# Kernel tuning notes

Hardware: AMD Instinct MI355X
Metric: run time of the kernel (lower is better)

## Reference

```python
import jax, jax.numpy as jnp
import numpy as np

N_NODES = 100000
N_EDGES = 1000000
D = 64  # gat_input_size == gat_hidden_size
NEG_SLOPE = 0.2  # PyG GATConv default leaky_relu slope


def setup_inputs() -> dict:
    key = jax.random.key(0)
    k1, k2, k3, k4, k5, k6 = jax.random.split(key, 6)
    g = jax.random.normal(k1, (N_NODES, D), dtype=jnp.float32)
    edge_index = jax.random.randint(k2, (2, N_EDGES), 0, N_NODES, dtype=jnp.int32)
    scale = 1.0 / np.sqrt(D)
    W = jax.random.normal(k3, (D, D), dtype=jnp.float32) * scale
    att_src = jax.random.normal(k4, (D,), dtype=jnp.float32) * scale
    att_dst = jax.random.normal(k5, (D,), dtype=jnp.float32) * scale
    bias = jnp.zeros((D,), dtype=jnp.float32)
    return {"g": g, "edge_index": edge_index, "W": W,
            "att_src": att_src, "att_dst": att_dst, "bias": bias}


def _gat_layer(x, src, dst, W, att_src, att_dst, bias):
    N = x.shape[0]
    h = x @ W                               # [N, D] projected features
    a_src = h @ att_src                     # [N] per-node source logits
    a_dst = h @ att_dst                     # [N] per-node target logits
    e = jax.nn.leaky_relu(a_src[src] + a_dst[dst], NEG_SLOPE)  # [E]
    # numerically stable segment softmax over edges grouped by target node
    m = jax.ops.segment_max(e, dst, num_segments=N)            # [N]
    m = jnp.where(jnp.isfinite(m), m, 0.0)                     # isolated nodes
    ex = jnp.exp(e - m[dst])                                   # [E]
    denom = jax.ops.segment_sum(ex, dst, num_segments=N)       # [N]
    alpha = ex / (denom[dst] + 1e-16)                          # [E]
    out = jax.ops.segment_sum(alpha[:, None] * h[src], dst, num_segments=N)
    return out + bias


def reference(g, edge_index, W, att_src, att_dst, bias):
    src, dst = edge_index[0], edge_index[1]
    for _ in range(4):  # same shared GAT applied 4 times
        g = _gat_layer(g, src, dst, W, att_src, att_dst, bias)
    return g
```

## Files before the change

kernel.cpp:

```cpp
#include <hip/hip_runtime.h>
#include <hip/hip_bf16.h>

typedef unsigned int u32;
typedef unsigned short u16;
typedef unsigned long long u64;
typedef __attribute__((ext_vector_type(8))) short short8;
typedef __attribute__((ext_vector_type(4))) float f32x4;
typedef __attribute__((ext_vector_type(2))) float f32x2;

#define LRELU_SLOPE 0.2f
#define BPB 32
#define MAXPER 13000

__device__ inline float bfbits(u32 hi) { union { u32 i; float f; } v; v.i = hi; return v.f; }
__device__ inline float bflo(u32 w) { return bfbits(w << 16); }
__device__ inline float bfhi(u32 w) { return bfbits(w & 0xFFFF0000u); }
__device__ inline float bf2f(u16 s) { return bfbits(((u32)s) << 16); }
__device__ inline u16 f2bf(float f) {
  union { float f; u32 i; } v; v.f = f;
  u32 r = v.i + 0x7FFFu + ((v.i >> 16) & 1u);
  return (u16)(r >> 16);
}
__device__ inline f32x2 up2(u32 w) { return (f32x2){bflo(w), bfhi(w)}; }

__global__ void dp_kernel(const u32* __restrict__ g, int nwords, int* __restrict__ mode,
                          const void* __restrict__ W, const void* __restrict__ as,
                          const void* __restrict__ ad, const void* __restrict__ bs,
                          float* __restrict__ pf, u16* __restrict__ wfrag,
                          int* __restrict__ gcnt) {
  __shared__ int cnt;
  if (threadIdx.x == 0) cnt = 0;
  if (threadIdx.x < 8) gcnt[threadIdx.x] = 0;
  __syncthreads();
  int c = 0;
  for (int i = threadIdx.x; i < nwords; i += 256) {
    u32 e = g[i] & 0x7F80u;
    if (e >= 0x3000u && e <= 0x4180u) c++;
  }
  atomicAdd(&cnt, c);
  __syncthreads();
  int md = (2 * cnt > nwords) ? 1 : 0;
  if (threadIdx.x == 0) *mode = md;

  for (int i = threadIdx.x; i < 4288; i += 256) {
    const void* p; int j;
    if (i < 4096)      { p = W;  j = i; }
    else if (i < 4160) { p = as; j = i - 4096; }
    else if (i < 4224) { p = ad; j = i - 4160; }
    else               { p = bs; j = i - 4224; }
    pf[i] = md ? bf2f(((const u16*)p)[j]) : ((const float*)p)[j];
  }
  __syncthreads();
  for (int i = threadIdx.x; i < 4096; i += 256) {
    int f = i >> 9, lane = (i >> 3) & 63, j = i & 7;
    int cc = f >> 1, t = f & 1;
    int k = 32 * t + 8 * (lane >> 4) + j;
    int n = 16 * cc + (lane & 15);
    wfrag[i] = f2bf(pf[k * 64 + n]);
  }
}

__global__ void __launch_bounds__(256) binA_kernel(
    const int* __restrict__ src, const int* __restrict__ dst, int* __restrict__ gcnt,
    uint2* __restrict__ binned, int E, int nper, int cap) {
  __shared__ int lcnt[8], lbase[8], lcur[8];
  const int K = 8;
  int tile0 = blockIdx.x * (256 * K);
  int t = threadIdx.x;
  if (t < 8) { lcnt[t] = 0; lcur[t] = 0; }
  __syncthreads();
  int dv[K], sv[K], bv[K];
#pragma unroll
  for (int j = 0; j < K; ++j) {
    int idx = tile0 + j * 256 + t;
    bool ok = idx < E;
    int d = ok ? __builtin_nontemporal_load(&dst[idx]) : 0;
    int s = ok ? __builtin_nontemporal_load(&src[idx]) : 0;
    int b = -1;
    if (ok) {
      b = (d >= 4 * nper) ? 4 : 0;
      if (d >= (b + 2) * nper) b += 2;
      if (d >= (b + 1) * nper) b += 1;
      atomicAdd(&lcnt[b], 1);
    }
    dv[j] = d; sv[j] = s; bv[j] = b;
  }
  __syncthreads();
  if (t < 8) lbase[t] = atomicAdd(&gcnt[t], lcnt[t]);
  __syncthreads();
#pragma unroll
  for (int j = 0; j < K; ++j) {
    int b = bv[j];
    if (b >= 0) {
      int slot = lbase[b] + atomicAdd(&lcur[b], 1);
      if (slot < cap) binned[(size_t)b * cap + slot] = make_uint2((u32)sv[j], (u32)dv[j]);
    }
  }
}

__global__ void __launch_bounds__(256) histA_kernel(
    const uint2* __restrict__ binned, const int* __restrict__ gcnt,
    u32* __restrict__ slices, int nper, int cap) {
  __shared__ u32 cnt_lds[MAXPER];
  int b = blockIdx.x & 7;
  int j = blockIdx.x >> 3;
  int cnt = gcnt[b]; if (cnt > cap) cnt = cap;
  int chunk = (cnt + BPB - 1) / BPB;
  int begin = j * chunk;
  int endc = begin + chunk; if (endc > cnt) endc = cnt;
  for (int k = threadIdx.x; k < nper; k += 256) cnt_lds[k] = 0;
  __syncthreads();
  const uint2* reg = binned + (size_t)b * cap;
  int kbase = b * nper;
  for (int i = begin + threadIdx.x; i < endc; i += 256)
    atomicAdd(&cnt_lds[(int)reg[i].y - kbase], 1u);
  __syncthreads();
  u32* out = slices + (size_t)(b * BPB + j) * nper;
  for (int k = threadIdx.x; k < nper; k += 256) out[k] = cnt_lds[k];
}

__global__ void scan1f_kernel(const u32* __restrict__ slices, int* __restrict__ row_off,
                              int* __restrict__ partials, int nper, int N) {
  __shared__ int smem[1024];
  int t = threadIdx.x;
  int idx = blockIdx.x * 1024 + t;
  int v = 0;
  if (idx < N) {
    int b = idx / nper;
    int kk = idx - b * nper;
    const u32* s = slices + (size_t)b * BPB * nper + kk;
    u32 tt = 0;
#pragma unroll 8
    for (int j = 0; j < BPB; ++j) tt += s[(size_t)j * nper];
    v = (int)((tt + 7u) & ~7u);
  }
  smem[t] = v;
  __syncthreads();
  for (int off = 1; off < 1024; off <<= 1) {
    int u = (t >= off) ? smem[t - off] : 0;
    __syncthreads();
    smem[t] += u;
    __syncthreads();
  }
  if (idx < N) row_off[idx + 1] = smem[t];
  if (t == 1023) partials[blockIdx.x] = smem[t];
}

__global__ void scan3c_kernel(int* __restrict__ row_off, const int* __restrict__ partials,
                              int P, u32* __restrict__ slices, int* __restrict__ csr_src,
                              int nper, int N, int dummy) {
  __shared__ int smem[1024];
  int t = threadIdx.x;
  int pv = (t < P) ? partials[t] : 0;
  smem[t] = pv;
  __syncthreads();
  for (int off = 1; off < 1024; off <<= 1) {
    int u = (t >= off) ? smem[t - off] : 0;
    __syncthreads();
    smem[t] += u;
    __syncthreads();
  }
  int blk = blockIdx.x;
  int prefix = (blk > 0) ? smem[blk - 1] : 0;
  int idx = blk * 1024 + t;
  if (idx == 0) row_off[0] = 0;
  if (idx < N) {
    int vend = row_off[idx + 1] + prefix;
    row_off[idx + 1] = vend;
    int b = idx / nper;
    int kk = idx - b * nper;
    u32* s = slices + (size_t)b * BPB * nper + kk;
    u32 tv[BPB];
    u32 deg = 0;
#pragma unroll
    for (int j = 0; j < BPB; ++j) { tv[j] = s[(size_t)j * nper]; deg += tv[j]; }
    u32 pdeg = (deg + 7u) & ~7u;
    u32 run = (u32)vend - pdeg;
#pragma unroll
    for (int j = 0; j < BPB; ++j) { s[(size_t)j * nper] = run; run += tv[j]; }
    for (u32 p = run; p < (u32)vend; ++p) csr_src[p] = dummy;
  }
}

__global__ void __launch_bounds__(256) scatterB_kernel(
    const uint2* __restrict__ binned, const int* __restrict__ gcnt,
    const u32* __restrict__ slices, int* __restrict__ csr_src, int nper, int cap) {
  __shared__ u32 base_lds[MAXPER];
  int b = blockIdx.x & 7;
  int j = blockIdx.x >> 3;
  int cnt = gcnt[b]; if (cnt > cap) cnt = cap;
  int chunk = (cnt + BPB - 1) / BPB;
  int begin = j * chunk;
  int endc = begin + chunk; if (endc > cnt) endc = cnt;
  const u32* s = slices + (size_t)(b * BPB + j) * nper;
  for (int k = threadIdx.x; k < nper; k += 256) base_lds[k] = s[k];
  __syncthreads();
  const uint2* reg = binned + (size_t)b * cap;
  int kbase = b * nper;
  for (int i = begin + threadIdx.x; i < endc; i += 256) {
    uint2 r = reg[i];
    u32 p = atomicAdd(&base_lds[(int)r.y - kbase], 1u);
    csr_src[p] = (int)r.x;
  }
}

__global__ void hist_local_kernel(const uint2* __restrict__ binned, const int* __restrict__ gcnt,
                                  int* __restrict__ deg, int cap) {
  int b = blockIdx.x & 7;
  int vb = blockIdx.x >> 3, nvb = gridDim.x >> 3;
  int cnt = gcnt[b]; if (cnt > cap) cnt = cap;
  const uint2* reg = binned + (size_t)b * cap;
  for (int i = vb * blockDim.x + threadIdx.x; i < cnt; i += nvb * blockDim.x)
    atomicAdd(&deg[reg[i].y], 1);
}

__global__ void scatter_local_kernel(const uint2* __restrict__ binned, const int* __restrict__ gcnt,
                                     int* __restrict__ cursor, int* __restrict__ csr_src, int cap) {
  int b = blockIdx.x & 7;
  int vb = blockIdx.x >> 3, nvb = gridDim.x >> 3;
  int cnt = gcnt[b]; if (cnt > cap) cnt = cap;
  const uint2* reg = binned + (size_t)b * cap;
  for (int i = vb * blockDim.x + threadIdx.x; i < cnt; i += nvb * blockDim.x) {
    uint2 r = reg[i];
    int p = atomicAdd(&cursor[r.y], 1);
    csr_src[p] = (int)r.x;
  }
}

__global__ void scan1_kernel(const int* __restrict__ deg, int* __restrict__ row_off,
                             int* __restrict__ partials, int N) {
  __shared__ int smem[1024];
  int t = threadIdx.x;
  int idx = blockIdx.x * 1024 + t;
  int v = (idx < N) ? (int)(((u32)deg[idx] + 7u) & ~7u) : 0;
  smem[t] = v;
  __syncthreads();
  for (int off = 1; off < 1024; off <<= 1) {
    int u = (t >= off) ? smem[t - off] : 0;
    __syncthreads();
    smem[t] += u;
    __syncthreads();
  }
  if (idx < N) row_off[idx + 1] = smem[t];
  if (t == 1023) partials[blockIdx.x] = smem[t];
}

__global__ void scan2_kernel(int* __restrict__ partials, int P) {
  __shared__ int smem[1024];
  int t = threadIdx.x;
  int v = (t < P) ? partials[t] : 0;
  smem[t] = v;
  __syncthreads();
  for (int off = 1; off < 1024; off <<= 1) {
    int u = (t >= off) ? smem[t - off] : 0;
    __syncthreads();
    smem[t] += u;
    __syncthreads();
  }
  if (t < P) partials[t] = smem[t];
}

__global__ void scan3_kernel(int* __restrict__ row_off, const int* __restrict__ partials,
                             int* __restrict__ cursor, int N) {
  int b = blockIdx.x;
  int idx = b * 1024 + threadIdx.x;
  if (idx < N) {
    int v = row_off[idx + 1] + ((b > 0) ? partials[b - 1] : 0);
    row_off[idx + 1] = v;
    if (idx + 1 < N) cursor[idx + 1] = v;
  }
  if (idx == 0) { row_off[0] = 0; cursor[0] = 0; }
}

__global__ void padC_kernel(const int* __restrict__ row_off, const int* __restrict__ cursor,
                            int* __restrict__ csr_src, int N, int dummy) {
  int i = blockIdx.x * blockDim.x + threadIdx.x;
  if (i >= N) return;
  int e = row_off[i + 1];
  for (int p = cursor[i]; p < e; ++p) csr_src[p] = dummy;
}

__global__ void __launch_bounds__(256) proj_mfma_kernel(
    const u16* __restrict__ x, const void* __restrict__ graw, const int* __restrict__ mode,
    int first, const u16* __restrict__ wfrag, const float* __restrict__ pf,
    u16* __restrict__ h, float* __restrict__ a_src, float* __restrict__ a_dst, int N) {
  if (blockIdx.x == 0) {
    if (threadIdx.x < 32) ((u32*)(h + (size_t)N * 64))[threadIdx.x] = 0u;
    else if (threadIdx.x == 32) a_src[N] = -1e30f;
  }
  int lane = threadIdx.x & 63;
  int quad = lane >> 4, m = lane & 15;
  int wtile = (int)((blockIdx.x * (size_t)blockDim.x + threadIdx.x) >> 6);
  int ntiles = (N + 15) >> 4;
  int nwaves = (int)((gridDim.x * (size_t)blockDim.x) >> 6);

  int md = *mode;
  bool f32in = (first && md == 0);
  const u16* xin = (first && md) ? (const u16*)graw : x;

  short8 bfrag[8];
#pragma unroll
  for (int f = 0; f < 8; ++f)
    bfrag[f] = *(const short8*)(wfrag + f * 512 + lane * 8);
  float asv[4], adv[4];
#pragma unroll
  for (int c = 0; c < 4; ++c) {
    asv[c] = pf[4096 + 16 * c + m];
    adv[c] = pf[4160 + 16 * c + m];
  }

  for (int tile = wtile; tile < ntiles; tile += nwaves) {
    int row0 = tile << 4;
    int rl = row0 + m; if (rl > N - 1) rl = N - 1;
    short8 a0, a1;
    if (f32in) {
      const float* xr = (const float*)graw + (size_t)rl * 64 + 8 * quad;
      float4 f0 = *(const float4*)(xr);
      float4 f1 = *(const float4*)(xr + 4);
      float4 f2 = *(const float4*)(xr + 32);
      float4 f3 = *(const float4*)(xr + 36);
      a0[0] = (short)f2bf(f0.x); a0[1] = (short)f2bf(f0.y);
      a0[2] = (short)f2bf(f0.z); a0[3] = (short)f2bf(f0.w);
      a0[4] = (short)f2bf(f1.x); a0[5] = (short)f2bf(f1.y);
      a0[6] = (short)f2bf(f1.z); a0[7] = (short)f2bf(f1.w);
      a1[0] = (short)f2bf(f2.x); a1[1] = (short)f2bf(f2.y);
      a1[2] = (short)f2bf(f2.z); a1[3] = (short)f2bf(f2.w);
      a1[4] = (short)f2bf(f3.x); a1[5] = (short)f2bf(f3.y);
      a1[6] = (short)f2bf(f3.z); a1[7] = (short)f2bf(f3.w);
    } else {
      const u16* xr = xin + (size_t)rl * 64 + 8 * quad;
      a0 = *(const short8*)(xr);
      a1 = *(const short8*)(xr + 32);
    }

    f32x4 acc[4];
#pragma unroll
    for (int c = 0; c < 4; ++c) {
      f32x4 z = {0.f, 0.f, 0.f, 0.f};
      z = __builtin_amdgcn_mfma_f32_16x16x32_bf16(a0, bfrag[2 * c + 0], z, 0, 0, 0);
      z = __builtin_amdgcn_mfma_f32_16x16x32_bf16(a1, bfrag[2 * c + 1], z, 0, 0, 0);
      acc[c] = z;
    }

#pragma unroll
    for (int r = 0; r < 4; ++r) {
      int row = row0 + 4 * quad + r;
      float v0 = acc[0][r], v1 = acc[1][r], v2 = acc[2][r], v3 = acc[3][r];
      if (row < N) {
        u16* hr = h + (size_t)row * 64 + m;
        hr[0]  = f2bf(v0);
        hr[16] = f2bf(v1);
        hr[32] = f2bf(v2);
        hr[48] = f2bf(v3);
      }
      float s1 = v0 * asv[0] + v1 * asv[1] + v2 * asv[2] + v3 * asv[3];
      float s2 = v0 * adv[0] + v1 * adv[1] + v2 * adv[2] + v3 * adv[3];
#pragma unroll
      for (int msk = 1; msk <= 8; msk <<= 1) {
        s1 += __shfl_xor(s1, msk, 64);
        s2 += __shfl_xor(s2, msk, 64);
      }
      if (m == 0 && row < N) { a_src[row] = s1; a_dst[row] = s2; }
    }
  }
}

__global__ void __launch_bounds__(256) gather_kernel(
    const u16* __restrict__ h, const float* __restrict__ a_src,
    const float* __restrict__ a_dst, const int* __restrict__ row_off,
    const int* __restrict__ csr_src, const float* __restrict__ pf,
    u16* __restrict__ xout, void* __restrict__ dout, int N, int last,
    const int* __restrict__ mode) {
  int lane = threadIdx.x & 63;
  int grp = lane >> 4;
  int eg  = (lane >> 3) & 1;
  int fg  = lane & 7;
  int wid = (int)((blockIdx.x * blockDim.x + threadIdx.x) >> 6);
  int i0 = wid * 4;
  if (i0 >= N) return;
  int i = i0 + grp;
  bool valid = i < N;

  int beg = 0, end = 0;
  float adv = 0.f;
  if (valid) {
    beg = row_off[i];
    end = row_off[i + 1];
    adv = a_dst[i];
  }

  f32x2 acc0 = {0.f, 0.f}, acc1 = {0.f, 0.f}, acc2 = {0.f, 0.f}, acc3 = {0.f, 0.f};
  float den = 0.f;

  for (int b0 = beg; b0 < end; b0 += 8) {
    int eA = b0 + eg;
    int sA = csr_src[eA];
    int sB = csr_src[eA + 2];
    int sC = csr_src[eA + 4];
    int sD = csr_src[eA + 6];
    float aA = a_src[sA];
    float aB = a_src[sB];
    float aC = a_src[sC];
    float aD = a_src[sD];
    uint4 hA = ((const uint4*)(h + (size_t)sA * 64))[fg];
    uint4 hB = ((const uint4*)(h + (size_t)sB * 64))[fg];
    uint4 hC = ((const uint4*)(h + (size_t)sC * 64))[fg];
    uint4 hD = ((const uint4*)(h + (size_t)sD * 64))[fg];

    float tA = aA + adv; tA = (tA > 0.f) ? tA : LRELU_SLOPE * tA;
    float tB = aB + adv; tB = (tB > 0.f) ? tB : LRELU_SLOPE * tB;
    float tC = aC + adv; tC = (tC > 0.f) ? tC : LRELU_SLOPE * tC;
    float tD = aD + adv; tD = (tD > 0.f) ? tD : LRELU_SLOPE * tD;
    float wA = __expf(fminf(tA, 60.f));
    float wB = __expf(fminf(tB, 60.f));
    float wC = __expf(fminf(tC, 60.f));
    float wD = __expf(fminf(tD, 60.f));
    den += (wA + wB) + (wC + wD);
    f32x2 wA2 = {wA, wA}, wB2 = {wB, wB}, wC2 = {wC, wC}, wD2 = {wD, wD};
    acc0 += wA2 * up2(hA.x); acc0 += wB2 * up2(hB.x);
    acc0 += wC2 * up2(hC.x); acc0 += wD2 * up2(hD.x);
    acc1 += wA2 * up2(hA.y); acc1 += wB2 * up2(hB.y);
    acc1 += wC2 * up2(hC.y); acc1 += wD2 * up2(hD.y);
    acc2 += wA2 * up2(hA.z); acc2 += wB2 * up2(hB.z);
    acc2 += wC2 * up2(hC.z); acc2 += wD2 * up2(hD.z);
    acc3 += wA2 * up2(hA.w); acc3 += wB2 * up2(hB.w);
    acc3 += wC2 * up2(hC.w); acc3 += wD2 * up2(hD.w);
  }

  den += __shfl_xor(den, 8, 64);
#pragma unroll
  for (int c = 0; c < 2; ++c) {
    acc0[c] += __shfl_xor(acc0[c], 8, 64);
    acc1[c] += __shfl_xor(acc1[c], 8, 64);
    acc2[c] += __shfl_xor(acc2[c], 8, 64);
    acc3[c] += __shfl_xor(acc3[c], 8, 64);
  }
  float inv = (den > 0.f) ? 1.f / den : 0.f;

  if (!valid || eg) return;

  float oa[8] = {acc0[0], acc0[1], acc1[0], acc1[1], acc2[0], acc2[1], acc3[0], acc3[1]};
  if (*mode || !last) {
    u32 o[4];
#pragma unroll
    for (int j = 0; j < 4; ++j) {
      float f0 = oa[2 * j]     * inv + pf[4224 + 8 * fg + 2 * j];
      float f1 = oa[2 * j + 1] * inv + pf[4224 + 8 * fg + 2 * j + 1];
      o[j] = (u32)f2bf(f0) | ((u32)f2bf(f1) << 16);
    }
    u16* base = last ? (u16*)dout : xout;
    *(uint4*)(base + (size_t)i * 64 + fg * 8) = make_uint4(o[0], o[1], o[2], o[3]);
  } else {
    float o[8];
#pragma unroll
    for (int j = 0; j < 8; ++j)
      o[j] = oa[j] * inv + pf[4224 + 8 * fg + j];
    float* dp = (float*)dout + (size_t)i * 64 + fg * 8;
    *(float4*)(dp)     = make_float4(o[0], o[1], o[2], o[3]);
    *(float4*)(dp + 4) = make_float4(o[4], o[5], o[6], o[7]);
  }
}

extern "C" void kernel_launch(void* const* d_in, const int* in_sizes, int n_in,
                              void* d_out, int out_size, void* d_ws, size_t ws_size,
                              hipStream_t stream) {
  const void* g     = d_in[0];
  const int*  edge  = (const int*)d_in[1];
  const void* Wp    = d_in[2];
  const void* attsp = d_in[3];
  const void* attdp = d_in[4];
  const void* biasp = d_in[5];

  const int D = 64;
  const int N = in_sizes[0] / D;
  const int E = in_sizes[1] / 2;
  const int* src = edge;
  const int* dst = edge + E;

  int nper = (N + 7) / 8;
  bool fast_csr = (nper <= MAXPER);

  char* ws = (char*)d_ws;
  size_t off = 0;
  auto alloc = [&](size_t bytes) -> char* {
    char* p = ws + off;
    off += (bytes + 255) & ~size_t(255);
    return p;
  };
  size_t h_bytes = (size_t)(N + 1) * D * sizeof(u16);
  size_t slice_bytes = (size_t)8 * BPB * nper * sizeof(u32);
  u16*   x        = (u16*)alloc((size_t)N * D * sizeof(u16));
  u16*   h        = (u16*)alloc(h_bytes > slice_bytes ? h_bytes : slice_bytes);
  u32*   slices   = (u32*)h;
  float* pf       = (float*)alloc(4288 * sizeof(float));
  u16*   wfrag    = (u16*)alloc(4096 * sizeof(u16));
  float* a_src    = (float*)alloc((size_t)(N + 1) * sizeof(float));
  float* a_dst    = (float*)alloc((size_t)N * sizeof(float));
  int*   deg      = (int*)alloc((size_t)N * sizeof(int));
  int*   row_off  = (int*)alloc((size_t)(N + 1) * sizeof(int));
  int*   cursor   = (int*)alloc((size_t)N * sizeof(int));
  int*   csr_src  = (int*)alloc(((size_t)E + 8 * (size_t)N) * sizeof(int));
  int*   partials = (int*)alloc(1024 * sizeof(int));
  int*   mode     = (int*)alloc(256);
  int*   gcnt     = (int*)alloc(256);
  int    cap      = E / 8 + 16384;
  uint2* binned   = (uint2*)alloc((size_t)8 * cap * sizeof(uint2));

  dp_kernel<<<1, 256, 0, stream>>>((const u32*)g, 4096, mode, Wp, attsp, attdp, biasp,
                                   pf, wfrag, gcnt);

  if (!fast_csr) hipMemsetAsync(deg, 0, (size_t)N * sizeof(int), stream);
  int abl = (E + 2047) / 2048;
  binA_kernel<<<abl, 256, 0, stream>>>(src, dst, gcnt, binned, E, nper, cap);

  int nblk = (N + 1023) / 1024;
  if (fast_csr) {
    histA_kernel<<<8 * BPB, 256, 0, stream>>>(binned, gcnt, slices, nper, cap);
    scan1f_kernel<<<nblk, 1024, 0, stream>>>(slices, row_off, partials, nper, N);
    scan3c_kernel<<<nblk, 1024, 0, stream>>>(row_off, partials, nblk, slices, csr_src,
                                             nper, N, N);
    scatterB_kernel<<<8 * BPB, 256, 0, stream>>>(binned, gcnt, slices, csr_src, nper, cap);
  } else {
    hist_local_kernel<<<1024, 256, 0, stream>>>(binned, gcnt, deg, cap);
    scan1_kernel<<<nblk, 1024, 0, stream>>>(deg, row_off, partials, N);
    scan2_kernel<<<1, 1024, 0, stream>>>(partials, nblk);
    scan3_kernel<<<nblk, 1024, 0, stream>>>(row_off, partials, cursor, N);
    scatter_local_kernel<<<1024, 256, 0, stream>>>(binned, gcnt, cursor, csr_src, cap);
    padC_kernel<<<(N + 255) / 256, 256, 0, stream>>>(row_off, cursor, csr_src, N, N);
  }

  int ntiles = (N + 15) / 16;
  int tblocks = (ntiles + 3) / 4;
  for (int layer = 0; layer < 4; ++layer) {
    proj_mfma_kernel<<<tblocks, 256, 0, stream>>>(x, g, mode, layer == 0 ? 1 : 0,
                                                  wfrag, pf, h, a_src, a_dst, N);
    int last = (layer == 3) ? 1 : 0;
    gather_kernel<<<(N + 15) / 16, 256, 0, stream>>>(h, a_src, a_dst, row_off, csr_src, pf,
                                                     x, d_out, N, last, mode);
  }
}
```

Before: 280.2 us.

## Fuse gather aggregation with next layer's projection using ping-pong buffers

```diff
diff --git a/kernel.cpp b/kernel.cpp
--- a/kernel.cpp
+++ b/kernel.cpp
@@ -280,13 +280,17 @@
   for (int p = cursor[i]; p < e; ++p) csr_src[p] = dummy;
 }
 
-__global__ void __launch_bounds__(256) proj_mfma_kernel(
-    const u16* __restrict__ x, const void* __restrict__ graw, const int* __restrict__ mode,
-    int first, const u16* __restrict__ wfrag, const float* __restrict__ pf,
-    u16* __restrict__ h, float* __restrict__ a_src, float* __restrict__ a_dst, int N) {
+__global__ void __launch_bounds__(256) proj0_kernel(
+    const void* __restrict__ graw, const int* __restrict__ mode,
+    const u16* __restrict__ wfrag, const float* __restrict__ pf,
+    u16* __restrict__ h0, u16* __restrict__ h1,
+    float* __restrict__ as0, float* __restrict__ as1,
+    float* __restrict__ ad0, int N) {
   if (blockIdx.x == 0) {
-    if (threadIdx.x < 32) ((u32*)(h + (size_t)N * 64))[threadIdx.x] = 0u;
-    else if (threadIdx.x == 32) a_src[N] = -1e30f;
+    if (threadIdx.x < 32)       ((u32*)(h0 + (size_t)N * 64))[threadIdx.x] = 0u;
+    else if (threadIdx.x < 64)  ((u32*)(h1 + (size_t)N * 64))[threadIdx.x - 32] = 0u;
+    else if (threadIdx.x == 64) as0[N] = -1e30f;
+    else if (threadIdx.x == 65) as1[N] = -1e30f;
   }
   int lane = threadIdx.x & 63;
   int quad = lane >> 4, m = lane & 15;
@@ -295,8 +299,7 @@
   int nwaves = (int)((gridDim.x * (size_t)blockDim.x) >> 6);
 
   int md = *mode;
-  bool f32in = (first && md == 0);
-  const u16* xin = (first && md) ? (const u16*)graw : x;
+  bool f32in = (md == 0);
 
   short8 bfrag[8];
 #pragma unroll
@@ -328,7 +331,7 @@
       a1[4] = (short)f2bf(f3.x); a1[5] = (short)f2bf(f3.y);
       a1[6] = (short)f2bf(f3.z); a1[7] = (short)f2bf(f3.w);
     } else {
-      const u16* xr = xin + (size_t)rl * 64 + 8 * quad;
+      const u16* xr = (const u16*)graw + (size_t)rl * 64 + 8 * quad;
       a0 = *(const short8*)(xr);
       a1 = *(const short8*)(xr + 32);
     }
@@ -347,7 +350,7 @@
       int row = row0 + 4 * quad + r;
       float v0 = acc[0][r], v1 = acc[1][r], v2 = acc[2][r], v3 = acc[3][r];
       if (row < N) {
-        u16* hr = h + (size_t)row * 64 + m;
+        u16* hr = h0 + (size_t)row * 64 + m;
         hr[0]  = f2bf(v0);
         hr[16] = f2bf(v1);
         hr[32] = f2bf(v2);
@@ -360,17 +363,136 @@
         s1 += __shfl_xor(s1, msk, 64);
         s2 += __shfl_xor(s2, msk, 64);
       }
-      if (m == 0 && row < N) { a_src[row] = s1; a_dst[row] = s2; }
-    }
-  }
-}
-
-__global__ void __launch_bounds__(256) gather_kernel(
+      if (m == 0 && row < N) { as0[row] = s1; ad0[row] = s2; }
+    }
+  }
+}
+
+__global__ void __launch_bounds__(256) fusedFG_kernel(
+    const u16* __restrict__ hin, const float* __restrict__ asi,
+    const float* __restrict__ adi, u16* __restrict__ hout,
+    float* __restrict__ aso, float* __restrict__ ado,
+    const int* __restrict__ row_off, const int* __restrict__ csr_src,
+    const float* __restrict__ pf, const u16* __restrict__ wfrag, int N) {
+  __shared__ u16 xs[16][72];
+  __shared__ float sred[2][16][4];
+
+  int tid = threadIdx.x;
+  int lane = tid & 63;
+  int w = tid >> 6;
+  int quad = lane >> 4, m = lane & 15;
+  int grp = lane >> 4;
+  int eg = (lane >> 3) & 1;
+  int fg = lane & 7;
+  int tile = blockIdx.x;
+  int row_in = w * 4 + grp;
+  int i = tile * 16 + row_in;
+  bool valid = i < N;
+
+  short8 bf0 = *(const short8*)(wfrag + (2 * w + 0) * 512 + lane * 8);
+  short8 bf1 = *(const short8*)(wfrag + (2 * w + 1) * 512 + lane * 8);
+  float asw = pf[4096 + 16 * w + m];
+  float adw = pf[4160 + 16 * w + m];
+
+  int beg = 0, end = 0;
+  float advv = 0.f;
+  if (valid) { beg = row_off[i]; end = row_off[i + 1]; advv = adi[i]; }
+
+  f32x2 acc0 = {0.f, 0.f}, acc1 = {0.f, 0.f}, acc2 = {0.f, 0.f}, acc3 = {0.f, 0.f};
+  float den = 0.f;
+  for (int b0 = beg; b0 < end; b0 += 8) {
+    int eA = b0 + eg;
+    int sA = csr_src[eA];
+    int sB = csr_src[eA + 2];
+    int sC = csr_src[eA + 4];
+    int sD = csr_src[eA + 6];
+    float aA = asi[sA];
+    float aB = asi[sB];
+    float aC = asi[sC];
+    float aD = asi[sD];
+    uint4 hA = ((const uint4*)(hin + (size_t)sA * 64))[fg];
+    uint4 hB = ((const uint4*)(hin + (size_t)sB * 64))[fg];
+    uint4 hC = ((const uint4*)(hin + (size_t)sC * 64))[fg];
+    uint4 hD = ((const uint4*)(hin + (size_t)sD * 64))[fg];
+
+    float tA = aA + advv; tA = (tA > 0.f) ? tA : LRELU_SLOPE * tA;
+    float tB = aB + advv; tB = (tB > 0.f) ? tB : LRELU_SLOPE * tB;
+    float tC = aC + advv; tC = (tC > 0.f) ? tC : LRELU_SLOPE * tC;
+    float tD = aD + advv; tD = (tD > 0.f) ? tD : LRELU_SLOPE * tD;
+    float wA = __expf(fminf(tA, 60.f));
+    float wB = __expf(fminf(tB, 60.f));
+    float wC = __expf(fminf(tC, 60.f));
+    float wD = __expf(fminf(tD, 60.f));
+    den += (wA + wB) + (wC + wD);
+    f32x2 wA2 = {wA, wA}, wB2 = {wB, wB}, wC2 = {wC, wC}, wD2 = {wD, wD};
+    acc0 += wA2 * up2(hA.x); acc0 += wB2 * up2(hB.x);
+    acc0 += wC2 * up2(hC.x); acc0 += wD2 * up2(hD.x);
+    acc1 += wA2 * up2(hA.y); acc1 += wB2 * up2(hB.y);
+    acc1 += wC2 * up2(hC.y); acc1 += wD2 * up2(hD.y);
+    acc2 += wA2 * up2(hA.z); acc2 += wB2 * up2(hB.z);
+    acc2 += wC2 * up2(hC.z); acc2 += wD2 * up2(hD.z);
+    acc3 += wA2 * up2(hA.w); acc3 += wB2 * up2(hB.w);
+    acc3 += wC2 * up2(hC.w); acc3 += wD2 * up2(hD.w);
+  }
+  den += __shfl_xor(den, 8, 64);
+#pragma unroll
+  for (int c = 0; c < 2; ++c) {
+    acc0[c] += __shfl_xor(acc0[c], 8, 64);
+    acc1[c] += __shfl_xor(acc1[c], 8, 64);
+    acc2[c] += __shfl_xor(acc2[c], 8, 64);
+    acc3[c] += __shfl_xor(acc3[c], 8, 64);
+  }
+  float inv = (den > 0.f) ? 1.f / den : 0.f;
+  float oa[8] = {acc0[0], acc0[1], acc1[0], acc1[1],
+                 acc2[0], acc2[1], acc3[0], acc3[1]};
+
+  if (!eg) {
+    u32 o[4];
+    if (valid) {
+#pragma unroll
+      for (int j = 0; j < 4; ++j) {
+        float v0 = oa[2 * j]     * inv + pf[4224 + 8 * fg + 2 * j];
+        float v1 = oa[2 * j + 1] * inv + pf[4224 + 8 * fg + 2 * j + 1];
+        o[j] = (u32)f2bf(v0) | ((u32)f2bf(v1) << 16);
+      }
+    } else {
+      o[0] = o[1] = o[2] = o[3] = 0u;
+    }
+    *(uint4*)&xs[row_in][fg * 8] = make_uint4(o[0], o[1], o[2], o[3]);
+  }
+  __syncthreads();
+
+  short8 a0 = *(const short8*)&xs[m][8 * quad];
+  short8 a1 = *(const short8*)&xs[m][32 + 8 * quad];
+  f32x4 z = {0.f, 0.f, 0.f, 0.f};
+  z = __builtin_amdgcn_mfma_f32_16x16x32_bf16(a0, bf0, z, 0, 0, 0);
+  z = __builtin_amdgcn_mfma_f32_16x16x32_bf16(a1, bf1, z, 0, 0, 0);
+#pragma unroll
+  for (int r = 0; r < 4; ++r) {
+    int row = tile * 16 + 4 * quad + r;
+    if (row < N) hout[(size_t)row * 64 + 16 * w + m] = f2bf(z[r]);
+    float s1 = z[r] * asw, s2 = z[r] * adw;
+#pragma unroll
+    for (int msk = 1; msk <= 8; msk <<= 1) {
+      s1 += __shfl_xor(s1, msk, 64);
+      s2 += __shfl_xor(s2, msk, 64);
+    }
+    if (m == 0) { sred[0][4 * quad + r][w] = s1; sred[1][4 * quad + r][w] = s2; }
+  }
+  __syncthreads();
+  if (tid < 32) {
+    int row = tid & 15, sel = tid >> 4;
+    float v = sred[sel][row][0] + sred[sel][row][1] + sred[sel][row][2] + sred[sel][row][3];
+    int gr = tile * 16 + row;
+    if (gr < N) (sel ? ado : aso)[gr] = v;
+  }
+}
+
+__global__ void __launch_bounds__(256) gatherL_kernel(
     const u16* __restrict__ h, const float* __restrict__ a_src,
     const float* __restrict__ a_dst, const int* __restrict__ row_off,
     const int* __restrict__ csr_src, const float* __restrict__ pf,
-    u16* __restrict__ xout, void* __restrict__ dout, int N, int last,
-    const int* __restrict__ mode) {
+    void* __restrict__ dout, int N, const int* __restrict__ mode) {
   int lane = threadIdx.x & 63;
   int grp = lane >> 4;
   int eg  = (lane >> 3) & 1;
@@ -440,7 +562,7 @@
   if (!valid || eg) return;
 
   float oa[8] = {acc0[0], acc0[1], acc1[0], acc1[1], acc2[0], acc2[1], acc3[0], acc3[1]};
-  if (*mode || !last) {
+  if (*mode) {
     u32 o[4];
 #pragma unroll
     for (int j = 0; j < 4; ++j) {
@@ -448,8 +570,7 @@
       float f1 = oa[2 * j + 1] * inv + pf[4224 + 8 * fg + 2 * j + 1];
       o[j] = (u32)f2bf(f0) | ((u32)f2bf(f1) << 16);
     }
-    u16* base = last ? (u16*)dout : xout;
-    *(uint4*)(base + (size_t)i * 64 + fg * 8) = make_uint4(o[0], o[1], o[2], o[3]);
+    *(uint4*)((u16*)dout + (size_t)i * 64 + fg * 8) = make_uint4(o[0], o[1], o[2], o[3]);
   } else {
     float o[8];
 #pragma unroll
@@ -489,13 +610,15 @@
   };
   size_t h_bytes = (size_t)(N + 1) * D * sizeof(u16);
   size_t slice_bytes = (size_t)8 * BPB * nper * sizeof(u32);
-  u16*   x        = (u16*)alloc((size_t)N * D * sizeof(u16));
-  u16*   h        = (u16*)alloc(h_bytes > slice_bytes ? h_bytes : slice_bytes);
-  u32*   slices   = (u32*)h;
+  u16*   h0       = (u16*)alloc(h_bytes > slice_bytes ? h_bytes : slice_bytes);
+  u16*   h1       = (u16*)alloc(h_bytes);
+  u32*   slices   = (u32*)h0;
   float* pf       = (float*)alloc(4288 * sizeof(float));
   u16*   wfrag    = (u16*)alloc(4096 * sizeof(u16));
-  float* a_src    = (float*)alloc((size_t)(N + 1) * sizeof(float));
-  float* a_dst    = (float*)alloc((size_t)N * sizeof(float));
+  float* as0      = (float*)alloc((size_t)(N + 1) * sizeof(float));
+  float* as1      = (float*)alloc((size_t)(N + 1) * sizeof(float));
+  float* ad0      = (float*)alloc((size_t)N * sizeof(float));
+  float* ad1      = (float*)alloc((size_t)N * sizeof(float));
   int*   deg      = (int*)alloc((size_t)N * sizeof(int));
   int*   row_off  = (int*)alloc((size_t)(N + 1) * sizeof(int));
   int*   cursor   = (int*)alloc((size_t)N * sizeof(int));
@@ -531,11 +654,16 @@
 
   int ntiles = (N + 15) / 16;
   int tblocks = (ntiles + 3) / 4;
-  for (int layer = 0; layer < 4; ++layer) {
-    proj_mfma_kernel<<<tblocks, 256, 0, stream>>>(x, g, mode, layer == 0 ? 1 : 0,
-                                                  wfrag, pf, h, a_src, a_dst, N);
-    int last = (layer == 3) ? 1 : 0;
-    gather_kernel<<<(N + 15) / 16, 256, 0, stream>>>(h, a_src, a_dst, row_off, csr_src, pf,
-                                                     x, d_out, N, last, mode);
-  }
-}
+
+  proj0_kernel<<<tblocks, 256, 0, stream>>>(g, mode, wfrag, pf, h0, h1, as0, as1, ad0, N);
+
+  fusedFG_kernel<<<ntiles, 256, 0, stream>>>(h0, as0, ad0, h1, as1, ad1,
+                                             row_off, csr_src, pf, wfrag, N);
+  fusedFG_kernel<<<ntiles, 256, 0, stream>>>(h1, as1, ad1, h0, as0, ad0,
+                                             row_off, csr_src, pf, wfrag, N);
+  fusedFG_kernel<<<ntiles, 256, 0, stream>>>(h0, as0, ad0, h1, as1, ad1,
+                                             row_off, csr_src, pf, wfrag, N);
+
+  gatherL_kernel<<<ntiles, 256, 0, stream>>>(h1, as1, ad1, row_off, csr_src, pf,
+                                             d_out, N, mode);
+}
```

Result: faster. 267.8 us (-4.4%).
